# Optimization experiments

Measured on AMD Instinct MI355X. Metric: run time of the kernel, lower is better.

The kernel has to match this reference:

```python
import jax, jax.numpy as jnp
import numpy as np
import math

B = 262144
STATE = 6
TOTAL_MEAS = 27
HID = 256
INPUT_DIM = TOTAL_MEAS * 2 + 1 + STATE + 12  # 73
PI = math.pi
NORM_R_SCALE = 500.0 / 150000.0
ANG_IDX = np.array([0, 1, 3, 4, 6, 9, 10, 12, 13, 15, 18, 19, 21, 22, 24])
ANG_MASK = np.zeros((TOTAL_MEAS,), dtype=bool)
ANG_MASK[ANG_IDX] = True


def setup_inputs() -> dict:
    key = jax.random.key(0)
    ks = jax.random.split(key, 16)
    s = lambda fan: 1.0 / math.sqrt(fan)
    inp = {
        "meas": jax.random.normal(ks[0], (B, TOTAL_MEAS), jnp.float32),
        "mask": jnp.ones((B, TOTAL_MEAS), jnp.float32),
        "dt": jax.random.uniform(ks[1], (B,), jnp.float32),
        "baselines": jax.random.normal(ks[2], (B, 12), jnp.float32),
        "x_prev": jax.random.normal(ks[3], (B, STATE), jnp.float32),
        "hx": jnp.zeros((B, HID), jnp.float32),
        # GRU params (torch gate order: r, z, n)
        "W_ih": jax.random.uniform(ks[4], (3 * HID, INPUT_DIM), jnp.float32, -s(HID), s(HID)),
        "W_hh": jax.random.uniform(ks[5], (3 * HID, HID), jnp.float32, -s(HID), s(HID)),
        "b_ih": jax.random.uniform(ks[6], (3 * HID,), jnp.float32, -s(HID), s(HID)),
        "b_hh": jax.random.uniform(ks[7], (3 * HID,), jnp.float32, -s(HID), s(HID)),
        # LayerNorm
        "ln_g": jnp.ones((HID,), jnp.float32),
        "ln_b": jnp.zeros((HID,), jnp.float32),
        # MLP head: 256 -> 256 -> 128 -> 6*27
        "W1": jax.random.uniform(ks[8], (256, HID), jnp.float32, -s(HID), s(HID)),
        "b1": jax.random.uniform(ks[9], (256,), jnp.float32, -s(HID), s(HID)),
        "W2": jax.random.uniform(ks[10], (128, 256), jnp.float32, -s(256), s(256)),
        "b2": jax.random.uniform(ks[11], (128,), jnp.float32, -s(256), s(256)),
        "W3": jax.random.uniform(ks[12], (STATE * TOTAL_MEAS, 128), jnp.float32, -s(128), s(128)),
        "b3": jax.random.uniform(ks[13], (STATE * TOTAL_MEAS,), jnp.float32, -s(128), s(128)),
    }
    return inp


def _wrap_angle(a):
    two_pi = 2.0 * PI
    return a - two_pi * jnp.round(a / two_pi)


def _platform_y_pred(x_rel):
    # x_rel: [B, 6] -> [B, 9] radar/EO measurement
    r_xy = jnp.sqrt(x_rel[:, 0] ** 2 + x_rel[:, 2] ** 2 + 1e-9)
    az = jnp.arctan2(x_rel[:, 2], x_rel[:, 0]) / PI
    el = jnp.arctan2(x_rel[:, 4], r_xy) / PI
    r = jnp.sqrt(x_rel[:, 0] ** 2 + x_rel[:, 2] ** 2 + x_rel[:, 4] ** 2 + 1e-9)
    z = jnp.zeros_like(r)
    return jnp.stack([az, el, r, az, el, z, az, z, z], axis=1)


def _forward(meas, mask, dt, baselines, x_prev, hx,
             W_ih, W_hh, b_ih, b_hh, ln_g, ln_b, W1, b1, W2, b2, W3, b3):
    # f_predict (CV model): x0 += dt*x1, x2 += dt*x3, x4 += dt*x5
    dt_scaled = dt * NORM_R_SCALE  # [B]
    zcol = jnp.zeros_like(x_prev[:, :1])
    shift = jnp.concatenate([x_prev[:, 1:2], zcol, x_prev[:, 3:4], zcol, x_prev[:, 5:6], zcol], axis=1)
    x_minus = x_prev + dt_scaled[:, None] * shift  # [B, 6]

    y_pred = jnp.concatenate([
        _platform_y_pred(x_minus),
        _platform_y_pred(x_minus - baselines[:, 0:6]),
        _platform_y_pred(x_minus - baselines[:, 6:12]),
    ], axis=1)  # [B, 27]

    innov = meas - y_pred
    wrapped = _wrap_angle(innov * PI) / PI
    innov = jnp.where(jnp.asarray(ANG_MASK)[None, :], wrapped, innov)
    innov = innov * mask

    rnn_in = jnp.concatenate([innov, mask, dt[:, None], x_minus, baselines], axis=1)  # [B, 73]

    # single-step GRU (torch semantics, gate order r,z,n)
    gi = rnn_in @ W_ih.T + b_ih  # [B, 3H]
    gh = hx @ W_hh.T + b_hh      # [B, 3H]
    gi_r, gi_z, gi_n = jnp.split(gi, 3, axis=1)
    gh_r, gh_z, gh_n = jnp.split(gh, 3, axis=1)
    r = jax.nn.sigmoid(gi_r + gh_r)
    z = jax.nn.sigmoid(gi_z + gh_z)
    n = jnp.tanh(gi_n + r * gh_n)
    h_new = (1.0 - z) * n + z * hx  # [B, H]

    # LayerNorm
    mu = jnp.mean(h_new, axis=-1, keepdims=True)
    var = jnp.var(h_new, axis=-1, keepdims=True)
    h_ln = (h_new - mu) / jnp.sqrt(var + 1e-5) * ln_g + ln_b

    # MLP gain head (dropout inactive at inference)
    f1 = jax.nn.relu(h_ln @ W1.T + b1)
    f2 = jax.nn.relu(f1 @ W2.T + b2)
    K = (f2 @ W3.T + b3).reshape(-1, STATE, TOTAL_MEAS)
    K = jnp.clip(K, -3.0, 3.0)

    correction = jnp.einsum('bsm,bm->bs', K, innov)
    x_new = jnp.clip(x_minus + correction, -5.0, 5.0)
    return x_new, h_new


def reference(meas, mask, dt, baselines, x_prev, hx,
              W_ih, W_hh, b_ih, b_hh, ln_g, ln_b, W1, b1, W2, b2, W3, b3):
    return _forward(meas, mask, dt, baselines, x_prev, hx,
                    W_ih, W_hh, b_ih, b_hh, ln_g, ln_b, W1, b1, W2, b2, W3, b3)
```

## Files before the change

kernel.cpp:

```cpp
#include <hip/hip_runtime.h>
#include <math.h>

#define B_TOTAL  262144
#define ROWS     64
#define NWG      (B_TOTAL/ROWS)
#define NTHR     512
#define PI_F     3.14159265358979323846f
#define NORM_R   (500.0f/150000.0f)

typedef float  f32x4  __attribute__((ext_vector_type(4)));
typedef short  bf16x8 __attribute__((ext_vector_type(8)));

#define GRU_SLAB 24576
#define OFF_GRU  0
#define OFF_W1   (11*GRU_SLAB)
#define OFF_W2   (OFF_W1 + 8*8192)
#define OFF_W3   (OFF_W2 + 8*4096)
#define W_TOTAL  (OFF_W3 + 4*8192)

#define LDS_RBF2  0
#define LDS_HB    17408
#define LDS_STG   (LDS_HB + 32768)
#define LDS_XMC   (LDS_STG + 2*49152)
#define LDS_LNS   (LDS_XMC + 1536)
#define LDS_TOTAL (LDS_LNS + 2048)

#define WAIT_VM0 asm volatile("s_waitcnt vmcnt(0)" ::: "memory")
#define BARv     __builtin_amdgcn_s_barrier()

__device__ __forceinline__ ushort f2bf(float f){
    union { float f; unsigned u; } v; v.f = f;
    unsigned r = v.u + 0x7FFFu + ((v.u >> 16) & 1u);
    return (ushort)(r >> 16);
}
__device__ __forceinline__ float b2f(ushort u){
    union { unsigned u; float f; } v; v.u = ((unsigned)u) << 16;
    return v.f;
}
__device__ __forceinline__ float sigm(float x){ return 1.0f/(1.0f+__expf(-x)); }
__device__ __forceinline__ float tanh_(float x){ return 1.0f - 2.0f/(__expf(2.0f*x)+1.0f); }
__device__ __forceinline__ int swzb(int row, int k){
    return ((row<<9) + (k<<1)) ^ ((row&7)<<4);
}
__device__ __forceinline__ bf16x8 rdW(const char* gb, int col, int lk){
    int slot = lk ^ ((col >> 1) & 3);
    return *(const bf16x8*)(gb + col*64 + slot*16);
}
template<int N>
__device__ __forceinline__ void stage_lin(const ushort* src, char* dst, int w, int lane){
    #pragma unroll
    for (int i = 0; i < N; ++i) {
        __builtin_amdgcn_global_load_lds(
            (const __attribute__((address_space(1))) void*)(src + (size_t)(i*512 + w*64 + lane)*8),
            (__attribute__((address_space(3))) void*)(dst + i*8192 + w*1024),
            16, 0, 0);
    }
}
__device__ __forceinline__ void mm4(const char* gb, int colbase, int lr, int lk,
                                    bf16x8 a0, bf16x8 a1, f32x4 acc[2][4]){
    #pragma unroll
    for (int j = 0; j < 4; ++j) {
        bf16x8 wf = rdW(gb, colbase + j*16 + lr, lk);
        acc[0][j] = __builtin_amdgcn_mfma_f32_16x16x32_bf16(wf, a0, acc[0][j], 0,0,0);
        acc[1][j] = __builtin_amdgcn_mfma_f32_16x16x32_bf16(wf, a1, acc[1][j], 0,0,0);
    }
}

__global__ void prep_weights(const float* __restrict__ W_ih, const float* __restrict__ W_hh,
                             const float* __restrict__ W1, const float* __restrict__ W2,
                             const float* __restrict__ W3, ushort* __restrict__ ws)
{
    int id = blockIdx.x*256 + threadIdx.x;
    if (id >= W_TOTAL) return;
    float v = 0.0f;
    if (id < OFF_W1) {
        int slab = id / GRU_SLAB, u = id % GRU_SLAB;
        int gate = u >> 13, u2 = u & 8191;
        int col = u2 >> 5, v5 = u2 & 31, slot = v5 >> 3, e = v5 & 7;
        int kq = slot ^ ((col >> 1) & 3);
        int k = slab*32 + kq*8 + e;
        int rowz = gate*256 + col;
        v = (k < 73) ? W_ih[rowz*73 + k] : ((k < 96) ? 0.0f : W_hh[rowz*256 + (k-96)]);
    } else if (id < OFF_W2) {
        int t = id - OFF_W1, kb = t >> 13, u2 = t & 8191;
        int col = u2 >> 5, v5 = u2 & 31, slot = v5 >> 3, e = v5 & 7;
        int kq = slot ^ ((col >> 1) & 3);
        v = W1[col*256 + kb*32 + kq*8 + e];
    } else if (id < OFF_W3) {
        int t = id - OFF_W2, kb = t >> 12, u2 = t & 4095;
        int col = u2 >> 5, v5 = u2 & 31, slot = v5 >> 3, e = v5 & 7;
        int kq = slot ^ ((col >> 1) & 3);
        v = W2[col*256 + kb*32 + kq*8 + e];
    } else {
        int t = id - OFF_W3, kb = t >> 13, u2 = t & 8191;
        int col = u2 >> 5, v5 = u2 & 31, slot = v5 >> 3, e = v5 & 7;
        int kq = slot ^ ((col >> 1) & 3);
        int k = kb*32 + kq*8 + e;
        v = (col < 162) ? W3[col*128 + k] : 0.0f;
    }
    ws[id] = f2bf(v);
}

__global__ __launch_bounds__(NTHR, 1) void knet_mfma(
    const float* __restrict__ meas, const float* __restrict__ mask,
    const float* __restrict__ dt,   const float* __restrict__ baselines,
    const float* __restrict__ x_prev, const float* __restrict__ hx,
    const float* __restrict__ b_ih, const float* __restrict__ b_hh,
    const float* __restrict__ ln_g, const float* __restrict__ ln_b,
    const float* __restrict__ b1,   const float* __restrict__ b2,
    const float* __restrict__ b3,
    const ushort* __restrict__ ws,
    float* __restrict__ out)
{
    extern __shared__ char smem[];
    ushort* Rbu  = (ushort*)(smem + LDS_RBF2);
    char*   Hb   = smem + LDS_HB;
    char*   STG  = smem + LDS_STG;
    float*  xmc  = (float*)(smem + LDS_XMC);
    float*  lnscr= (float*)(smem + LDS_LNS);

    const int tid  = threadIdx.x;
    const int w    = __builtin_amdgcn_readfirstlane(tid >> 6);
    const int nq   = w & 3;
    const int mh   = w >> 2;
    const int lane = tid & 63;
    const int lr   = lane & 15;
    const int lk   = lane >> 4;
    const int lk8  = lk * 8;
    const int row0 = blockIdx.x * ROWS;
    const int mrow = mh*32 + lr;
    float* hout = out + (size_t)B_TOTAL*6;

    stage_lin<6>(ws + OFF_GRU, STG, w, lane);

    float* scr = (float*)(STG + 49152);
    {
        const size_t m0 = (size_t)row0*27;
        for (int i = tid; i < 1728; i += NTHR) scr[i]        = meas[m0 + i];
        for (int i = tid; i < 1728; i += NTHR) scr[1728 + i] = mask[m0 + i];
        const size_t b0 = (size_t)row0*12;
        for (int i = tid; i < 768; i += NTHR)  scr[3456 + i] = baselines[b0 + i];
        if (tid < 384) scr[4224 + tid] = x_prev[(size_t)row0*6 + tid];
        if (tid < 64)  scr[4608 + tid] = dt[row0 + tid];
        const size_t hbase = (size_t)row0 * 256;
        #pragma unroll
        for (int ii = 0; ii < 4; ++ii) {
            int cid = tid + ii*NTHR;
            int r  = cid >> 5;
            int k0 = (cid & 31) << 3;
            const float4* p = (const float4*)(hx + hbase + (size_t)r*256 + k0);
            float4 u = p[0], v2 = p[1];
            bf16x8 o;
            o[0]=(short)f2bf(u.x);  o[1]=(short)f2bf(u.y);  o[2]=(short)f2bf(u.z);  o[3]=(short)f2bf(u.w);
            o[4]=(short)f2bf(v2.x); o[5]=(short)f2bf(v2.y); o[6]=(short)f2bf(v2.z); o[7]=(short)f2bf(v2.w);
            *(bf16x8*)(Hb + swzb(r, k0)) = o;
        }
    }
    __syncthreads();

    if (w < 4) {
        const int row = lane;
        const float dtv = scr[4608 + row];
        const float dts = dtv * NORM_R;
        float xp[6], xm[6];
        #pragma unroll
        for (int s = 0; s < 6; ++s) xp[s] = scr[4224 + row*6 + s];
        xm[0] = xp[0] + dts*xp[1]; xm[1] = xp[1];
        xm[2] = xp[2] + dts*xp[3]; xm[3] = xp[3];
        xm[4] = xp[4] + dts*xp[5]; xm[5] = xp[5];
        if (w < 3) {
            float xr[6];
            #pragma unroll
            for (int s = 0; s < 6; ++s) {
                float b = (w == 0) ? 0.0f : scr[3456 + row*12 + (w-1)*6 + s];
                xr[s] = xm[s] - b;
            }
            float rxy = sqrtf(xr[0]*xr[0] + xr[2]*xr[2] + 1e-9f);
            float azv = atan2f(xr[2], xr[0]) * (1.0f/PI_F);
            float elv = atan2f(xr[4], rxy)   * (1.0f/PI_F);
            float rrv = sqrtf(xr[0]*xr[0] + xr[2]*xr[2] + xr[4]*xr[4] + 1e-9f);
            float y[9] = {azv, elv, rrv, azv, elv, 0.0f, azv, 0.0f, 0.0f};
            const bool ang[9] = {true,true,false,true,true,false,true,false,false};
            #pragma unroll
            for (int i = 0; i < 9; ++i) {
                int m = w*9 + i;
                float ms = scr[1728 + row*27 + m];
                float v  = scr[row*27 + m] - y[i];
                if (ang[i]) v = v - 2.0f*rintf(v*0.5f);
                v *= ms;
                Rbu[row*104 + m]      = f2bf(v);
                Rbu[row*104 + 27 + m] = f2bf(ms);
            }
        } else {
            Rbu[row*104 + 54] = f2bf(dtv);
            #pragma unroll
            for (int s = 0; s < 6; ++s) Rbu[row*104 + 55 + s] = f2bf(xm[s]);
            #pragma unroll
            for (int q = 0; q < 12; ++q) Rbu[row*104 + 61 + q] = f2bf(scr[3456 + row*12 + q]);
            #pragma unroll
            for (int k = 73; k < 96; ++k) Rbu[row*104 + k] = 0;
            #pragma unroll
            for (int s = 0; s < 6; ++s) xmc[row*6 + s] = xm[s];
        }
    }
    __syncthreads();

    f32x4 ar[2][4], az[2][4], agi[2][4], agh[2][4];
    #pragma unroll
    for (int i = 0; i < 2; ++i)
        #pragma unroll
        for (int j = 0; j < 4; ++j) {
            ar[i][j]=(f32x4){0,0,0,0}; az[i][j]=(f32x4){0,0,0,0};
            agi[i][j]=(f32x4){0,0,0,0}; agh[i][j]=(f32x4){0,0,0,0};
        }
    #pragma unroll
    for (int kb = 0; kb < 11; ++kb) {
        WAIT_VM0; BARv;
        if (kb < 10) stage_lin<6>(ws + OFF_GRU + (kb+1)*GRU_SLAB, STG + ((kb+1)&1)*49152, w, lane);
        else         stage_lin<6>(ws + OFF_W1,                    STG + 49152,            w, lane);
        const char* sb = STG + (kb&1)*49152;
        bf16x8 a0, a1;
        if (kb < 3) { a0 = *(const bf16x8*)(Rbu + mrow*104 + kb*32 + lk8);
                      a1 = *(const bf16x8*)(Rbu + (mrow+16)*104 + kb*32 + lk8); }
        else        { a0 = *(const bf16x8*)(Hb + swzb(mrow,    (kb-3)*32 + lk8));
                      a1 = *(const bf16x8*)(Hb + swzb(mrow+16, (kb-3)*32 + lk8)); }
        __builtin_amdgcn_s_setprio(1);
        mm4(sb,         nq*64, lr, lk, a0, a1, ar);
        mm4(sb + 16384, nq*64, lr, lk, a0, a1, az);
        if (kb < 3) mm4(sb + 32768, nq*64, lr, lk, a0, a1, agi);
        else        mm4(sb + 32768, nq*64, lr, lk, a0, a1, agh);
        __builtin_amdgcn_s_setprio(0);
    }

    f32x4 hnv[2][4];
    float lsum[2] = {0,0}, lsq[2] = {0,0};
    #pragma unroll
    for (int j = 0; j < 4; ++j) {
        const int c0 = nq*64 + j*16 + lk*4;
        f32x4 bir = *(const f32x4*)(b_ih + c0),        bhr = *(const f32x4*)(b_hh + c0);
        f32x4 biz = *(const f32x4*)(b_ih + 256 + c0),  bhz = *(const f32x4*)(b_hh + 256 + c0);
        f32x4 bin_= *(const f32x4*)(b_ih + 512 + c0),  bhn = *(const f32x4*)(b_hh + 512 + c0);
        #pragma unroll
        for (int i = 0; i < 2; ++i) {
            const int row = mh*32 + i*16 + lr;
            uint2 hxd = *(const uint2*)(Hb + swzb(row, c0));
            float hx_[4] = { b2f((ushort)(hxd.x & 0xffffu)), b2f((ushort)(hxd.x >> 16)),
                             b2f((ushort)(hxd.y & 0xffffu)), b2f((ushort)(hxd.y >> 16)) };
            f32x4 hn4;
            #pragma unroll
            for (int e = 0; e < 4; ++e) {
                float rg = sigm(ar[i][j][e] + bir[e] + bhr[e]);
                float zg = sigm(az[i][j][e] + biz[e] + bhz[e]);
                float ng = tanh_(agi[i][j][e] + bin_[e] + rg*(agh[i][j][e] + bhn[e]));
                float hn = (1.0f - zg)*ng + zg*hx_[e];
                hn4[e] = hn;
                lsum[i] += hn; lsq[i] += hn*hn;
            }
            hnv[i][j] = hn4;
            float4 st = { hn4[0], hn4[1], hn4[2], hn4[3] };
            *(float4*)(hout + (size_t)(row0+row)*256 + c0) = st;
        }
    }
    #pragma unroll
    for (int i = 0; i < 2; ++i) {
        lsum[i] += __shfl_xor(lsum[i], 16); lsum[i] += __shfl_xor(lsum[i], 32);
        lsq[i]  += __shfl_xor(lsq[i], 16);  lsq[i]  += __shfl_xor(lsq[i], 32);
    }
    if (lk == 0) {
        #pragma unroll
        for (int i = 0; i < 2; ++i) {
            const int row = mh*32 + i*16 + lr;
            lnscr[row*8 + nq*2 + 0] = lsum[i];
            lnscr[row*8 + nq*2 + 1] = lsq[i];
        }
    }
    __syncthreads();

    {
        float mu[2], rstd[2];
        #pragma unroll
        for (int i = 0; i < 2; ++i) {
            const int row = mh*32 + i*16 + lr;
            float s = 0, q = 0;
            #pragma unroll
            for (int qq = 0; qq < 4; ++qq) { s += lnscr[row*8 + qq*2]; q += lnscr[row*8 + qq*2 + 1]; }
            mu[i] = s * (1.0f/256.0f);
            rstd[i] = rsqrtf(q*(1.0f/256.0f) - mu[i]*mu[i] + 1e-5f);
        }
        #pragma unroll
        for (int j = 0; j < 4; ++j) {
            const int c0 = nq*64 + j*16 + lk*4;
            f32x4 g4 = *(const f32x4*)(ln_g + c0);
            f32x4 b4 = *(const f32x4*)(ln_b + c0);
            #pragma unroll
            for (int i = 0; i < 2; ++i) {
                const int row = mh*32 + i*16 + lr;
                float v0 = (hnv[i][j][0]-mu[i])*rstd[i]*g4[0] + b4[0];
                float v1 = (hnv[i][j][1]-mu[i])*rstd[i]*g4[1] + b4[1];
                float v2 = (hnv[i][j][2]-mu[i])*rstd[i]*g4[2] + b4[2];
                float v3 = (hnv[i][j][3]-mu[i])*rstd[i]*g4[3] + b4[3];
                uint2 o;
                o.x = (unsigned)f2bf(v0) | ((unsigned)f2bf(v1) << 16);
                o.y = (unsigned)f2bf(v2) | ((unsigned)f2bf(v3) << 16);
                *(uint2*)(Hb + swzb(row, c0)) = o;
            }
        }
    }
    __syncthreads();

    f32x4 c2[2][4];
    #pragma unroll
    for (int i = 0; i < 2; ++i)
        #pragma unroll
        for (int j = 0; j < 4; ++j) c2[i][j] = (f32x4){0,0,0,0};
    WAIT_VM0; BARv;
    stage_lin<6>(ws + OFF_W1 + 3*8192, STG, w, lane);
    {
        const char* sb = STG + 49152;
        #pragma unroll
        for (int kb = 0; kb < 3; ++kb) {
            bf16x8 a0 = *(const bf16x8*)(Hb + swzb(mrow,    kb*32 + lk8));
            bf16x8 a1 = *(const bf16x8*)(Hb + swzb(mrow+16, kb*32 + lk8));
            __builtin_amdgcn_s_setprio(1);
            mm4(sb + kb*16384, nq*64, lr, lk, a0, a1, c2);
            __builtin_amdgcn_s_setprio(0);
        }
    }
    WAIT_VM0; BARv;
    stage_lin<4>(ws + OFF_W1 + 6*8192, STG + 49152, w, lane);
    {
        const char* sb = STG;
        #pragma unroll
        for (int kb = 3; kb < 6; ++kb) {
            bf16x8 a0 = *(const bf16x8*)(Hb + swzb(mrow,    kb*32 + lk8));
            bf16x8 a1 = *(const bf16x8*)(Hb + swzb(mrow+16, kb*32 + lk8));
            __builtin_amdgcn_s_setprio(1);
            mm4(sb + (kb-3)*16384, nq*64, lr, lk, a0, a1, c2);
            __builtin_amdgcn_s_setprio(0);
        }
    }
    WAIT_VM0; BARv;
    stage_lin<4>(ws + OFF_W2, STG, w, lane);
    {
        const char* sb = STG + 49152;
        #pragma unroll
        for (int kb = 6; kb < 8; ++kb) {
            bf16x8 a0 = *(const bf16x8*)(Hb + swzb(mrow,    kb*32 + lk8));
            bf16x8 a1 = *(const bf16x8*)(Hb + swzb(mrow+16, kb*32 + lk8));
            __builtin_amdgcn_s_setprio(1);
            mm4(sb + (kb-6)*16384, nq*64, lr, lk, a0, a1, c2);
            __builtin_amdgcn_s_setprio(0);
        }
    }
    __syncthreads();
    #pragma unroll
    for (int j = 0; j < 4; ++j) {
        const int c0 = nq*64 + j*16 + lk*4;
        f32x4 b4 = *(const f32x4*)(b1 + c0);
        #pragma unroll
        for (int i = 0; i < 2; ++i) {
            const int row = mh*32 + i*16 + lr;
            uint2 o;
            o.x = (unsigned)f2bf(fmaxf(c2[i][j][0]+b4[0],0.f)) | ((unsigned)f2bf(fmaxf(c2[i][j][1]+b4[1],0.f)) << 16);
            o.y = (unsigned)f2bf(fmaxf(c2[i][j][2]+b4[2],0.f)) | ((unsigned)f2bf(fmaxf(c2[i][j][3]+b4[3],0.f)) << 16);
            *(uint2*)(Hb + swzb(row, c0)) = o;
        }
    }
    __syncthreads();

    f32x4 c3[2][2];
    #pragma unroll
    for (int i = 0; i < 2; ++i)
        #pragma unroll
        for (int j = 0; j < 2; ++j) c3[i][j] = (f32x4){0,0,0,0};
    WAIT_VM0; BARv;
    stage_lin<4>(ws + OFF_W2 + 4*4096, STG + 49152, w, lane);
    {
        const char* sb = STG;
        #pragma unroll
        for (int kb = 0; kb < 4; ++kb) {
            bf16x8 a0 = *(const bf16x8*)(Hb + swzb(mrow,    kb*32 + lk8));
            bf16x8 a1 = *(const bf16x8*)(Hb + swzb(mrow+16, kb*32 + lk8));
            __builtin_amdgcn_s_setprio(1);
            #pragma unroll
            for (int j = 0; j < 2; ++j) {
                bf16x8 wf = rdW(sb + kb*8192, nq*32 + j*16 + lr, lk);
                c3[0][j] = __builtin_amdgcn_mfma_f32_16x16x32_bf16(wf, a0, c3[0][j], 0,0,0);
                c3[1][j] = __builtin_amdgcn_mfma_f32_16x16x32_bf16(wf, a1, c3[1][j], 0,0,0);
            }
            __builtin_amdgcn_s_setprio(0);
        }
    }
    WAIT_VM0; BARv;
    stage_lin<4>(ws + OFF_W3, STG, w, lane);
    {
        const char* sb = STG + 49152;
        #pragma unroll
        for (int kb = 4; kb < 8; ++kb) {
            bf16x8 a0 = *(const bf16x8*)(Hb + swzb(mrow,    kb*32 + lk8));
            bf16x8 a1 = *(const bf16x8*)(Hb + swzb(mrow+16, kb*32 + lk8));
            __builtin_amdgcn_s_setprio(1);
            #pragma unroll
            for (int j = 0; j < 2; ++j) {
                bf16x8 wf = rdW(sb + (kb-4)*8192, nq*32 + j*16 + lr, lk);
                c3[0][j] = __builtin_amdgcn_mfma_f32_16x16x32_bf16(wf, a0, c3[0][j], 0,0,0);
                c3[1][j] = __builtin_amdgcn_mfma_f32_16x16x32_bf16(wf, a1, c3[1][j], 0,0,0);
            }
            __builtin_amdgcn_s_setprio(0);
        }
    }
    f32x4 iv[2][3];
    #pragma unroll
    for (int j = 0; j < 3; ++j) {
        #pragma unroll
        for (int i = 0; i < 2; ++i) {
            const int row = mh*32 + i*16 + lr;
            #pragma unroll
            for (int e = 0; e < 4; ++e) {
                int col = nq*48 + j*16 + lk*4 + e;
                int m = col - 27*(col/27);
                iv[i][j][e] = b2f(Rbu[row*104 + m]);
            }
        }
    }
    __syncthreads();
    #pragma unroll
    for (int j = 0; j < 2; ++j) {
        const int c0 = nq*32 + j*16 + lk*4;
        f32x4 b4 = *(const f32x4*)(b2 + c0);
        #pragma unroll
        for (int i = 0; i < 2; ++i) {
            const int row = mh*32 + i*16 + lr;
            uint2 o;
            o.x = (unsigned)f2bf(fmaxf(c3[i][j][0]+b4[0],0.f)) | ((unsigned)f2bf(fmaxf(c3[i][j][1]+b4[1],0.f)) << 16);
            o.y = (unsigned)f2bf(fmaxf(c3[i][j][2]+b4[2],0.f)) | ((unsigned)f2bf(fmaxf(c3[i][j][3]+b4[3],0.f)) << 16);
            *(uint2*)((char*)Rbu + row*272 + c0*2) = o;
        }
    }
    __syncthreads();

    f32x4 c4[2][3];
    #pragma unroll
    for (int i = 0; i < 2; ++i)
        #pragma unroll
        for (int j = 0; j < 3; ++j) c4[i][j] = (f32x4){0,0,0,0};
    WAIT_VM0; BARv;
    stage_lin<4>(ws + OFF_W3 + 2*8192, STG + 49152, w, lane);
    {
        const char* sb = STG;
        #pragma unroll
        for (int kb = 0; kb < 2; ++kb) {
            bf16x8 a0 = *(const bf16x8*)((char*)Rbu + (mrow     )*272 + (kb*32 + lk8)*2);
            bf16x8 a1 = *(const bf16x8*)((char*)Rbu + (mrow + 16)*272 + (kb*32 + lk8)*2);
            __builtin_amdgcn_s_setprio(1);
            #pragma unroll
            for (int j = 0; j < 3; ++j) {
                bf16x8 wf = rdW(sb + kb*16384, nq*48 + j*16 + lr, lk);
                c4[0][j] = __builtin_amdgcn_mfma_f32_16x16x32_bf16(wf, a0, c4[0][j], 0,0,0);
                c4[1][j] = __builtin_amdgcn_mfma_f32_16x16x32_bf16(wf, a1, c4[1][j], 0,0,0);
            }
            __builtin_amdgcn_s_setprio(0);
        }
    }
    WAIT_VM0; BARv;
    {
        const char* sb = STG + 49152;
        #pragma unroll
        for (int kb = 2; kb < 4; ++kb) {
            bf16x8 a0 = *(const bf16x8*)((char*)Rbu + (mrow     )*272 + (kb*32 + lk8)*2);
            bf16x8 a1 = *(const bf16x8*)((char*)Rbu + (mrow + 16)*272 + (kb*32 + lk8)*2);
            __builtin_amdgcn_s_setprio(1);
            #pragma unroll
            for (int j = 0; j < 3; ++j) {
                bf16x8 wf = rdW(sb + (kb-2)*16384, nq*48 + j*16 + lr, lk);
                c4[0][j] = __builtin_amdgcn_mfma_f32_16x16x32_bf16(wf, a0, c4[0][j], 0,0,0);
                c4[1][j] = __builtin_amdgcn_mfma_f32_16x16x32_bf16(wf, a1, c4[1][j], 0,0,0);
            }
            __builtin_amdgcn_s_setprio(0);
        }
    }
    #pragma unroll
    for (int j = 0; j < 3; ++j) {
        #pragma unroll
        for (int i = 0; i < 2; ++i) {
            const int row = mh*32 + i*16 + lr;
            #pragma unroll
            for (int e = 0; e < 4; ++e) {
                int col = nq*48 + j*16 + lk*4 + e;
                if (col < 162) {
                    int s = col / 27;
                    float K = fminf(fmaxf(c4[i][j][e] + b3[col], -3.0f), 3.0f);
                    atomicAdd(&xmc[row*6 + s], K * iv[i][j][e]);
                }
            }
        }
    }
    __syncthreads();

    for (int t = tid; t < ROWS*6; t += NTHR) {
        int row = t / 6, s = t - row*6;
        float v = fminf(fmaxf(xmc[t], -5.0f), 5.0f);
        out[(size_t)(row0+row)*6 + s] = v;
    }
}

extern "C" void kernel_launch(void* const* d_in, const int* in_sizes, int n_in,
                              void* d_out, int out_size, void* d_ws, size_t ws_size,
                              hipStream_t stream) {
    const float* meas      = (const float*)d_in[0];
    const float* mask      = (const float*)d_in[1];
    const float* dtv       = (const float*)d_in[2];
    const float* baselines = (const float*)d_in[3];
    const float* x_prev    = (const float*)d_in[4];
    const float* hx        = (const float*)d_in[5];
    const float* W_ih      = (const float*)d_in[6];
    const float* W_hh      = (const float*)d_in[7];
    const float* b_ih      = (const float*)d_in[8];
    const float* b_hh      = (const float*)d_in[9];
    const float* ln_g      = (const float*)d_in[10];
    const float* ln_b      = (const float*)d_in[11];
    const float* W1        = (const float*)d_in[12];
    const float* b1        = (const float*)d_in[13];
    const float* W2        = (const float*)d_in[14];
    const float* b2        = (const float*)d_in[15];
    const float* W3        = (const float*)d_in[16];
    const float* b3        = (const float*)d_in[17];
    ushort* wsb = (ushort*)d_ws;
    float* outp = (float*)d_out;

    prep_weights<<<(W_TOTAL + 255)/256, 256, 0, stream>>>(W_ih, W_hh, W1, W2, W3, wsb);
    knet_mfma<<<NWG, NTHR, LDS_TOTAL, stream>>>(
        meas, mask, dtv, baselines, x_prev, hx,
        b_ih, b_hh, ln_g, ln_b, b1, b2, b3, wsb, outp);
}
```

Baseline: 693.0 us.

## Repartition GRU GEMM warps to cover all 64 rows and 32 columns each

Changes the GRU-stage warp tiling so that each of the 8 waves owns all 64 batch rows and a 32-column slice of each gate. Previously each wave held 32 rows by 64 columns. Each weight fragment read from LDS is now reused across four row tiles instead of two, which halves per-wave weight LDS reads at the cost of loading four activation fragments. The LayerNorm partial-sum scratch grows to 8 per-wave slots per row, and the LDS allocation grows to match.

```diff
diff --git a/kernel.cpp b/kernel.cpp
--- a/kernel.cpp
+++ b/kernel.cpp
@@ -23,7 +23,7 @@
 #define LDS_STG   (LDS_HB + 32768)
 #define LDS_XMC   (LDS_STG + 2*49152)
 #define LDS_LNS   (LDS_XMC + 1536)
-#define LDS_TOTAL (LDS_LNS + 2048)
+#define LDS_TOTAL (LDS_LNS + 4096)
 
 #define WAIT_VM0 asm volatile("s_waitcnt vmcnt(0)" ::: "memory")
 #define BARv     __builtin_amdgcn_s_barrier()
@@ -63,6 +63,16 @@
         bf16x8 wf = rdW(gb, colbase + j*16 + lr, lk);
         acc[0][j] = __builtin_amdgcn_mfma_f32_16x16x32_bf16(wf, a0, acc[0][j], 0,0,0);
         acc[1][j] = __builtin_amdgcn_mfma_f32_16x16x32_bf16(wf, a1, acc[1][j], 0,0,0);
+    }
+}
+__device__ __forceinline__ void mmG(const char* gb, int colbase, int lr, int lk,
+                                    const bf16x8 a[4], f32x4 acc[4][2]){
+    #pragma unroll
+    for (int j = 0; j < 2; ++j) {
+        bf16x8 wf = rdW(gb, colbase + j*16 + lr, lk);
+        #pragma unroll
+        for (int i = 0; i < 4; ++i)
+            acc[i][j] = __builtin_amdgcn_mfma_f32_16x16x32_bf16(wf, a[i], acc[i][j], 0,0,0);
     }
 }
 
@@ -129,6 +139,7 @@
     const int lk8  = lk * 8;
     const int row0 = blockIdx.x * ROWS;
     const int mrow = mh*32 + lr;
+    const int cw   = w * 32;
     float* hout = out + (size_t)B_TOTAL*6;
 
     stage_lin<6>(ws + OFF_GRU, STG, w, lane);
@@ -205,11 +216,11 @@
     }
     __syncthreads();
 
-    f32x4 ar[2][4], az[2][4], agi[2][4], agh[2][4];
-    #pragma unroll
-    for (int i = 0; i < 2; ++i)
-        #pragma unroll
-        for (int j = 0; j < 4; ++j) {
+    f32x4 ar[4][2], az[4][2], agi[4][2], agh[4][2];
+    #pragma unroll
+    for (int i = 0; i < 4; ++i)
+        #pragma unroll
+        for (int j = 0; j < 2; ++j) {
             ar[i][j]=(f32x4){0,0,0,0}; az[i][j]=(f32x4){0,0,0,0};
             agi[i][j]=(f32x4){0,0,0,0}; agh[i][j]=(f32x4){0,0,0,0};
         }
@@ -219,30 +230,35 @@
         if (kb < 10) stage_lin<6>(ws + OFF_GRU + (kb+1)*GRU_SLAB, STG + ((kb+1)&1)*49152, w, lane);
         else         stage_lin<6>(ws + OFF_W1,                    STG + 49152,            w, lane);
         const char* sb = STG + (kb&1)*49152;
-        bf16x8 a0, a1;
-        if (kb < 3) { a0 = *(const bf16x8*)(Rbu + mrow*104 + kb*32 + lk8);
-                      a1 = *(const bf16x8*)(Rbu + (mrow+16)*104 + kb*32 + lk8); }
-        else        { a0 = *(const bf16x8*)(Hb + swzb(mrow,    (kb-3)*32 + lk8));
-                      a1 = *(const bf16x8*)(Hb + swzb(mrow+16, (kb-3)*32 + lk8)); }
+        bf16x8 a[4];
+        if (kb < 3) {
+            #pragma unroll
+            for (int i = 0; i < 4; ++i)
+                a[i] = *(const bf16x8*)(Rbu + (i*16 + lr)*104 + kb*32 + lk8);
+        } else {
+            #pragma unroll
+            for (int i = 0; i < 4; ++i)
+                a[i] = *(const bf16x8*)(Hb + swzb(i*16 + lr, (kb-3)*32 + lk8));
+        }
         __builtin_amdgcn_s_setprio(1);
-        mm4(sb,         nq*64, lr, lk, a0, a1, ar);
-        mm4(sb + 16384, nq*64, lr, lk, a0, a1, az);
-        if (kb < 3) mm4(sb + 32768, nq*64, lr, lk, a0, a1, agi);
-        else        mm4(sb + 32768, nq*64, lr, lk, a0, a1, agh);
+        mmG(sb,         cw, lr, lk, a, ar);
+        mmG(sb + 16384, cw, lr, lk, a, az);
+        if (kb < 3) mmG(sb + 32768, cw, lr, lk, a, agi);
+        else        mmG(sb + 32768, cw, lr, lk, a, agh);
         __builtin_amdgcn_s_setprio(0);
     }
 
-    f32x4 hnv[2][4];
-    float lsum[2] = {0,0}, lsq[2] = {0,0};
-    #pragma unroll
-    for (int j = 0; j < 4; ++j) {
-        const int c0 = nq*64 + j*16 + lk*4;
+    f32x4 hnv[4][2];
+    float lsum[4] = {0,0,0,0}, lsq[4] = {0,0,0,0};
+    #pragma unroll
+    for (int j = 0; j < 2; ++j) {
+        const int c0 = cw + j*16 + lk*4;
         f32x4 bir = *(const f32x4*)(b_ih + c0),        bhr = *(const f32x4*)(b_hh + c0);
         f32x4 biz = *(const f32x4*)(b_ih + 256 + c0),  bhz = *(const f32x4*)(b_hh + 256 + c0);
         f32x4 bin_= *(const f32x4*)(b_ih + 512 + c0),  bhn = *(const f32x4*)(b_hh + 512 + c0);
         #pragma unroll
-        for (int i = 0; i < 2; ++i) {
-            const int row = mh*32 + i*16 + lr;
+        for (int i = 0; i < 4; ++i) {
+            const int row = i*16 + lr;
             uint2 hxd = *(const uint2*)(Hb + swzb(row, c0));
             float hx_[4] = { b2f((ushort)(hxd.x & 0xffffu)), b2f((ushort)(hxd.x >> 16)),
                              b2f((ushort)(hxd.y & 0xffffu)), b2f((ushort)(hxd.y >> 16)) };
@@ -262,39 +278,39 @@
         }
     }
     #pragma unroll
-    for (int i = 0; i < 2; ++i) {
+    for (int i = 0; i < 4; ++i) {
         lsum[i] += __shfl_xor(lsum[i], 16); lsum[i] += __shfl_xor(lsum[i], 32);
         lsq[i]  += __shfl_xor(lsq[i], 16);  lsq[i]  += __shfl_xor(lsq[i], 32);
     }
     if (lk == 0) {
         #pragma unroll
-        for (int i = 0; i < 2; ++i) {
-            const int row = mh*32 + i*16 + lr;
-            lnscr[row*8 + nq*2 + 0] = lsum[i];
-            lnscr[row*8 + nq*2 + 1] = lsq[i];
-        }
-    }
-    __syncthreads();
-
-    {
-        float mu[2], rstd[2];
-        #pragma unroll
-        for (int i = 0; i < 2; ++i) {
-            const int row = mh*32 + i*16 + lr;
+        for (int i = 0; i < 4; ++i) {
+            const int row = i*16 + lr;
+            lnscr[row*16 + w*2 + 0] = lsum[i];
+            lnscr[row*16 + w*2 + 1] = lsq[i];
+        }
+    }
+    __syncthreads();
+
+    {
+        float mu[4], rstd[4];
+        #pragma unroll
+        for (int i = 0; i < 4; ++i) {
+            const int row = i*16 + lr;
             float s = 0, q = 0;
             #pragma unroll
-            for (int qq = 0; qq < 4; ++qq) { s += lnscr[row*8 + qq*2]; q += lnscr[row*8 + qq*2 + 1]; }
+            for (int ww = 0; ww < 8; ++ww) { s += lnscr[row*16 + ww*2]; q += lnscr[row*16 + ww*2 + 1]; }
             mu[i] = s * (1.0f/256.0f);
             rstd[i] = rsqrtf(q*(1.0f/256.0f) - mu[i]*mu[i] + 1e-5f);
         }
         #pragma unroll
-        for (int j = 0; j < 4; ++j) {
-            const int c0 = nq*64 + j*16 + lk*4;
+        for (int j = 0; j < 2; ++j) {
+            const int c0 = cw + j*16 + lk*4;
             f32x4 g4 = *(const f32x4*)(ln_g + c0);
             f32x4 b4 = *(const f32x4*)(ln_b + c0);
             #pragma unroll
-            for (int i = 0; i < 2; ++i) {
-                const int row = mh*32 + i*16 + lr;
+            for (int i = 0; i < 4; ++i) {
+                const int row = i*16 + lr;
                 float v0 = (hnv[i][j][0]-mu[i])*rstd[i]*g4[0] + b4[0];
                 float v1 = (hnv[i][j][1]-mu[i])*rstd[i]*g4[1] + b4[1];
                 float v2 = (hnv[i][j][2]-mu[i])*rstd[i]*g4[2] + b4[2];
```

Measured after the change: 738.9 us. +6.6%, slower.
